# Performance work log

Measured on AMD Instinct MI355X. Metric: run time of the kernel, lower is better.

The kernel has to match this reference:

```python
import jax, jax.numpy as jnp
import numpy as np

COMMITMENT_COST = 0.25


def setup_inputs() -> dict:
    key = jax.random.key(0)
    k1, k2 = jax.random.split(key)
    # z_latents: [B, H, W, D] encoder output latents
    z_latents = jax.random.normal(k1, (128, 32, 32, 64), dtype=jnp.float32)
    # embeddings: [D, K] codebook, uniform init like tf.random_uniform_initializer (default [-0.05, 0.05])
    embeddings = jax.random.uniform(k2, (64, 1024), dtype=jnp.float32, minval=-0.05, maxval=0.05)
    return {"z_latents": z_latents, "embeddings": embeddings}


def reference(z_latents, embeddings):
    d, k = embeddings.shape
    flat = z_latents.reshape(-1, d)  # [N, D]
    # squared L2 distances to each codebook entry: [N, K]
    distances = (
        jnp.sum(flat * flat, axis=1, keepdims=True)
        - 2.0 * (flat @ embeddings)
        + jnp.sum(embeddings * embeddings, axis=0, keepdims=True)
    )
    # argmax(-d) == argmin(d) (both take first occurrence on ties)
    encoding_indices = jnp.argmin(distances, axis=1)  # [N]
    # one-hot @ embeddings.T is just a gather of codebook rows
    quantized = jnp.take(embeddings.T, encoding_indices, axis=0).reshape(z_latents.shape)
    commitment_loss = jnp.mean((jax.lax.stop_gradient(quantized) - z_latents) ** 2)
    embedding_loss = jnp.mean((jax.lax.stop_gradient(z_latents) - quantized) ** 2)
    vq_loss = embedding_loss + COMMITMENT_COST * commitment_loss
    # straight-through estimator
    quantized_st = z_latents + jax.lax.stop_gradient(quantized - z_latents)
    return quantized_st, vq_loss
```

## Files before the change

### kernel.cpp

```cpp
#include <hip/hip_runtime.h>

#pragma clang fp contract(off)

typedef __attribute__((ext_vector_type(8))) short short8;
typedef __attribute__((ext_vector_type(4))) float f32x4;

#define MARGIN 0.02f

static __device__ __forceinline__ unsigned short f2b(float f) {
    union { float f; unsigned u; } x; x.f = f;
    unsigned u = x.u;
    return (unsigned short)((u + 0x7FFFu + ((u >> 16) & 1u)) >> 16);
}

template <int ES>
static __device__ __forceinline__ float np_dist(
    const float* __restrict__ zr, const float* __restrict__ ecol,
    float zn, float en) {
    float c = 0.f;
    #pragma unroll
    for (int i = 0; i < 64; ++i) c = fmaf(zr[i], ecol[i * ES], c);
    float t = zn - 2.f * c;
    return t + en;
}

__global__ __launch_bounds__(256) void vq_prep_t(
    const float* __restrict__ E, float* __restrict__ Et) {
    int t = blockIdx.x * 256 + threadIdx.x;
    int k = t >> 6, d = t & 63;
    Et[t] = E[d * 1024 + k];
}

template <int ES>
__global__ __launch_bounds__(256) void vq_prep(
    const float* __restrict__ src, float* __restrict__ ws_loss,
    float* __restrict__ enorm) {
    int c = blockIdx.x * 256 + threadIdx.x;
    const float* col = src + (ES == 1 ? c * 64 : c);
    float s2 = 0.f;
    #pragma unroll
    for (int d = 0; d < 64; ++d) {
        float v = col[d * ES];
        s2 = fmaf(v, v, s2);
    }
    enorm[c] = s2;
    if (c == 0) *ws_loss = 0.f;
}

template <bool USE_ET>
__global__ __launch_bounds__(256) void vq_main(
    const float* __restrict__ z, const float* __restrict__ E,
    const float* __restrict__ Et, const float* __restrict__ enorm,
    float* __restrict__ ws_loss, float* __restrict__ out) {
    __shared__ unsigned short sB[128 * 64];
    __shared__ float sEn[1024];
    __shared__ float sZn[128];
    __shared__ int sIdx[128];
    __shared__ float sRed[4];

    const int tid = threadIdx.x;
    const int w = tid >> 6;
    const int l = tid & 63;
    const int quad = l >> 4;
    const int m = l & 15;
    const int b = blockIdx.x;

    ((float4*)sEn)[tid] = ((const float4*)enorm)[tid];

    if (tid < 128) {
        const float* zr = z + (b * 128 + tid) * 64;
        float S[16];
        #pragma unroll
        for (int u = 0; u < 16; ++u) { float v = zr[u]; S[u] = v * v; }
        #pragma unroll
        for (int t = 1; t < 4; ++t)
            #pragma unroll
            for (int u = 0; u < 16; ++u) {
                float v = zr[16 * t + u];
                float sq = v * v;
                S[u] = S[u] + sq;
            }
        float R0 = (S[0] + S[4]) + (S[8] + S[12]);
        float R1 = (S[1] + S[5]) + (S[9] + S[13]);
        float R2 = (S[2] + S[6]) + (S[10] + S[14]);
        float R3 = (S[3] + S[7]) + (S[11] + S[15]);
        sZn[tid] = (R0 + R1) + (R2 + R3);
    }

    short8 a[2][2];
    #pragma unroll
    for (int rt = 0; rt < 2; ++rt) {
        const int rowl = w * 32 + rt * 16 + m;
        #pragma unroll
        for (int s = 0; s < 2; ++s) {
            const float* zp = z + (b * 128 + rowl) * 64 + s * 32 + quad * 8;
            union { float4 v; float f[4]; } u0, u1;
            u0.v = *(const float4*)zp;
            u1.v = *(const float4*)(zp + 4);
            short8 av;
            #pragma unroll
            for (int j = 0; j < 4; ++j) av[j] = (short)f2b(u0.f[j]);
            #pragma unroll
            for (int j = 0; j < 4; ++j) av[4 + j] = (short)f2b(u1.f[j]);
            a[rt][s] = av;
        }
    }

    float v1[2][4], v2[2][4];
    int k1[2][4], k2[2][4];
    #pragma unroll
    for (int rt = 0; rt < 2; ++rt)
        #pragma unroll
        for (int r = 0; r < 4; ++r) {
            v1[rt][r] = 3.4e38f; v2[rt][r] = 3.4e38f;
            k1[rt][r] = 0; k2[rt][r] = 0;
        }

    for (int st = 0; st < 8; ++st) {
        #pragma unroll
        for (int i = 0; i < 4; ++i) {
            const int u = tid + i * 256;
            const int d0 = (u & 31) * 2;
            const int cg = u >> 5;
            const float* e0 = E + d0 * 1024 + st * 128 + cg * 4;
            union { float4 v; float f[4]; } va, vb;
            va.v = *(const float4*)e0;
            vb.v = *(const float4*)(e0 + 1024);
            #pragma unroll
            for (int j = 0; j < 4; ++j) {
                const int col = cg * 4 + j;
                const unsigned lo = f2b(va.f[j]);
                const unsigned hi = f2b(vb.f[j]);
                const int gi = col * 8 + ((d0 >> 3) ^ (col & 7));
                *(unsigned*)&sB[gi * 8 + (d0 & 7)] = lo | (hi << 16);
            }
        }
        __syncthreads();

        #pragma unroll
        for (int ct = 0; ct < 8; ++ct) {
            const int c = st * 8 + ct;
            const int colb = (ct * 16 + m) * 8;
            short8 b0 = *(const short8*)&sB[(colb + (quad ^ (m & 7))) * 8];
            short8 b1 = *(const short8*)&sB[(colb + ((4 + quad) ^ (m & 7))) * 8];
            f32x4 acc0 = {0.f, 0.f, 0.f, 0.f};
            f32x4 acc1 = {0.f, 0.f, 0.f, 0.f};
            acc0 = __builtin_amdgcn_mfma_f32_16x16x32_bf16(a[0][0], b0, acc0, 0, 0, 0);
            acc0 = __builtin_amdgcn_mfma_f32_16x16x32_bf16(a[0][1], b1, acc0, 0, 0, 0);
            acc1 = __builtin_amdgcn_mfma_f32_16x16x32_bf16(a[1][0], b0, acc1, 0, 0, 0);
            acc1 = __builtin_amdgcn_mfma_f32_16x16x32_bf16(a[1][1], b1, acc1, 0, 0, 0);
            const float en = sEn[c * 16 + m];
            #pragma unroll
            for (int r = 0; r < 4; ++r) {
                float v0 = fmaf(-2.f, acc0[r], en);
                bool p1 = v0 < v1[0][r];
                bool p2 = v0 < v2[0][r];
                v2[0][r] = p1 ? v1[0][r] : (p2 ? v0 : v2[0][r]);
                k2[0][r] = p1 ? k1[0][r] : (p2 ? c : k2[0][r]);
                v1[0][r] = p1 ? v0 : v1[0][r];
                k1[0][r] = p1 ? c : k1[0][r];
                float w1 = fmaf(-2.f, acc1[r], en);
                bool q1 = w1 < v1[1][r];
                bool q2 = w1 < v2[1][r];
                v2[1][r] = q1 ? v1[1][r] : (q2 ? w1 : v2[1][r]);
                k2[1][r] = q1 ? k1[1][r] : (q2 ? c : k2[1][r]);
                v1[1][r] = q1 ? w1 : v1[1][r];
                k1[1][r] = q1 ? c : k1[1][r];
            }
        }
        __syncthreads();
    }

    float la = 0.f;
    #pragma unroll
    for (int rt = 0; rt < 2; ++rt) {
        #pragma unroll
        for (int r = 0; r < 4; ++r) {
            float vb = v1[rt][r];
            #pragma unroll
            for (int mask = 1; mask <= 8; mask <<= 1)
                vb = fminf(vb, __shfl_xor(vb, mask));
            const int rowl = w * 32 + rt * 16 + quad * 4 + r;
            const float zn = sZn[rowl];
            const float* zr = z + (b * 128 + rowl) * 64;
            float d = 3.4e38f;
            int kk = 0x7fffffff;
            if (v1[rt][r] <= vb + MARGIN) {
                kk = k1[rt][r] * 16 + m;
                d = USE_ET ? np_dist<1>(zr, Et + kk * 64, zn, sEn[kk])
                           : np_dist<1024>(zr, E + kk, zn, sEn[kk]);
            }
            if (v2[rt][r] <= vb + MARGIN) {
                int kc = k2[rt][r] * 16 + m;
                float dd = USE_ET ? np_dist<1>(zr, Et + kc * 64, zn, sEn[kc])
                                  : np_dist<1024>(zr, E + kc, zn, sEn[kc]);
                if (dd < d || (dd == d && kc < kk)) { d = dd; kk = kc; }
            }
            #pragma unroll
            for (int mask = 1; mask <= 8; mask <<= 1) {
                float d2 = __shfl_xor(d, mask);
                int c2 = __shfl_xor(kk, mask);
                bool take = (d2 < d) || (d2 == d && c2 < kk);
                d = take ? d2 : d;
                kk = take ? c2 : kk;
            }
            if (m == 0) {
                sIdx[rowl] = kk;
                la += d;
            }
        }
    }
    __syncthreads();

    {
        const int row_local = w * 32 + (l >> 1);
        const int half = l & 1;
        const int idx = sIdx[row_local];
        union { float s[32]; float4 f[8]; } tmp;
        if (USE_ET) {
            const float4* src = (const float4*)(Et + idx * 64 + half * 32);
            #pragma unroll
            for (int q4 = 0; q4 < 8; ++q4) tmp.f[q4] = src[q4];
        } else {
            #pragma unroll
            for (int dd = 0; dd < 32; ++dd) tmp.s[dd] = E[(half * 32 + dd) * 1024 + idx];
        }
        float4* dst = (float4*)(out + (b * 128 + row_local) * 64 + half * 32);
        #pragma unroll
        for (int q4 = 0; q4 < 8; ++q4) dst[q4] = tmp.f[q4];
    }

    #pragma unroll
    for (int mask = 32; mask >= 1; mask >>= 1) la += __shfl_xor(la, mask);
    if (l == 0) sRed[w] = la;
    __syncthreads();
    if (tid == 0) atomicAdd(ws_loss, sRed[0] + sRed[1] + sRed[2] + sRed[3]);
}

__global__ void vq_final(const float* __restrict__ ws_loss,
                         float* __restrict__ out) {
    out[8388608] = (*ws_loss) * (1.25f / 8388608.f);
}

extern "C" void kernel_launch(void* const* d_in, const int* in_sizes, int n_in,
                              void* d_out, int out_size, void* d_ws, size_t ws_size,
                              hipStream_t stream) {
    const float* z = (const float*)d_in[0];
    const float* E = (const float*)d_in[1];
    float* out = (float*)d_out;

    char* ws = (char*)d_ws;
    float* loss = (float*)ws;
    float* enorm = (float*)(ws + 128);
    float* Et = (float*)(ws + 8192);
    const bool useEt = ws_size >= (size_t)(8192 + 65536 * 4);

    if (useEt) {
        vq_prep_t<<<256, 256, 0, stream>>>(E, Et);
        vq_prep<1><<<4, 256, 0, stream>>>(Et, loss, enorm);
        vq_main<true><<<1024, 256, 0, stream>>>(z, E, Et, enorm, loss, out);
    } else {
        vq_prep<1024><<<4, 256, 0, stream>>>(E, loss, enorm);
        vq_main<false><<<1024, 256, 0, stream>>>(z, E, Et, enorm, loss, out);
    }
    vq_final<<<1, 1, 0, stream>>>(loss, out);
}
```

Before: 174.8 us.

## Precompute swizzled bf16 codebook, double-buffer LDS tiles, pack index into distance bits

A single fused prep kernel now builds the transposed fp32 codebook, the norms, and a pre-swizzled bf16 copy of the codebook. Each main-kernel block then streams the bf16 copy straight into double-buffered shared memory, with the next tile prefetched into registers while MFMAs run. This removes the per-block fp32 load and bf16 conversion and one barrier per stage. The top-2 tracking packs the 6-bit column-tile index into the low mantissa bits of the distance, so fminf and fmed3 replace compare/select chains; this costs a little precision in the candidate screen, which the margin-based exact recheck absorbs. Shared memory doubles for sB, which may lower occupancy.

```diff
diff --git a/kernel.cpp b/kernel.cpp
--- a/kernel.cpp
+++ b/kernel.cpp
@@ -24,35 +24,49 @@
     return t + en;
 }
 
-__global__ __launch_bounds__(256) void vq_prep_t(
-    const float* __restrict__ E, float* __restrict__ Et) {
-    int t = blockIdx.x * 256 + threadIdx.x;
-    int k = t >> 6, d = t & 63;
-    Et[t] = E[d * 1024 + k];
-}
-
-template <int ES>
-__global__ __launch_bounds__(256) void vq_prep(
-    const float* __restrict__ src, float* __restrict__ ws_loss,
-    float* __restrict__ enorm) {
-    int c = blockIdx.x * 256 + threadIdx.x;
-    const float* col = src + (ES == 1 ? c * 64 : c);
-    float s2 = 0.f;
-    #pragma unroll
-    for (int d = 0; d < 64; ++d) {
-        float v = col[d * ES];
-        s2 = fmaf(v, v, s2);
-    }
-    enorm[c] = s2;
-    if (c == 0) *ws_loss = 0.f;
-}
-
-template <bool USE_ET>
+template <bool ET, bool EB>
+__global__ __launch_bounds__(256) void vq_prep_all(
+    const float* __restrict__ E, float* __restrict__ ws_loss,
+    float* __restrict__ enorm, float* __restrict__ Et,
+    unsigned* __restrict__ EbW) {
+    const int t = blockIdx.x * 256 + threadIdx.x;
+    if (ET) {
+        Et[t] = E[(t & 63) * 1024 + (t >> 6)];
+    }
+    if (EB) {
+        if (t < 32768) {
+            const int st = t >> 12;
+            const int r = t & 4095;
+            const int col = r >> 5;
+            const int w = r & 31;
+            const int g = w >> 2;
+            const int d0 = ((g ^ (col & 7)) << 3) | ((w & 3) << 1);
+            const int gc = st * 128 + col;
+            const unsigned lo = f2b(E[d0 * 1024 + gc]);
+            const unsigned hi = f2b(E[(d0 + 1) * 1024 + gc]);
+            EbW[t] = lo | (hi << 16);
+        }
+    }
+    if (t < 1024) {
+        const float* colp = E + t;
+        float s2 = 0.f;
+        #pragma unroll
+        for (int d = 0; d < 64; ++d) {
+            float v = colp[d * 1024];
+            s2 = fmaf(v, v, s2);
+        }
+        enorm[t] = s2;
+        if (t == 0) *ws_loss = 0.f;
+    }
+}
+
+template <bool USE_ET, bool USE_EB>
 __global__ __launch_bounds__(256) void vq_main(
     const float* __restrict__ z, const float* __restrict__ E,
-    const float* __restrict__ Et, const float* __restrict__ enorm,
+    const float* __restrict__ Et, const unsigned short* __restrict__ Eb,
+    const float* __restrict__ enorm,
     float* __restrict__ ws_loss, float* __restrict__ out) {
-    __shared__ unsigned short sB[128 * 64];
+    __shared__ unsigned short sB[2][128 * 64];
     __shared__ float sEn[1024];
     __shared__ float sZn[128];
     __shared__ int sIdx[128];
@@ -106,43 +120,61 @@
         }
     }
 
-    float v1[2][4], v2[2][4];
-    int k1[2][4], k2[2][4];
+    float v1p[2][4], v2p[2][4];
     #pragma unroll
     for (int rt = 0; rt < 2; ++rt)
         #pragma unroll
-        for (int r = 0; r < 4; ++r) {
-            v1[rt][r] = 3.4e38f; v2[rt][r] = 3.4e38f;
-            k1[rt][r] = 0; k2[rt][r] = 0;
-        }
+        for (int r = 0; r < 4; ++r) { v1p[rt][r] = 3.4e38f; v2p[rt][r] = 3.4e38f; }
+
+    short8 nx0, nx1, nx2, nx3;
+    if (USE_EB) {
+        const short8* s0 = (const short8*)Eb;
+        short8* dp = (short8*)sB[0];
+        #pragma unroll
+        for (int i = 0; i < 4; ++i) dp[tid + i * 256] = s0[tid + i * 256];
+        __syncthreads();
+    }
 
     for (int st = 0; st < 8; ++st) {
-        #pragma unroll
-        for (int i = 0; i < 4; ++i) {
-            const int u = tid + i * 256;
-            const int d0 = (u & 31) * 2;
-            const int cg = u >> 5;
-            const float* e0 = E + d0 * 1024 + st * 128 + cg * 4;
-            union { float4 v; float f[4]; } va, vb;
-            va.v = *(const float4*)e0;
-            vb.v = *(const float4*)(e0 + 1024);
-            #pragma unroll
-            for (int j = 0; j < 4; ++j) {
-                const int col = cg * 4 + j;
-                const unsigned lo = f2b(va.f[j]);
-                const unsigned hi = f2b(vb.f[j]);
-                const int gi = col * 8 + ((d0 >> 3) ^ (col & 7));
-                *(unsigned*)&sB[gi * 8 + (d0 & 7)] = lo | (hi << 16);
-            }
-        }
-        __syncthreads();
+        const unsigned short* sBc;
+        if (USE_EB) {
+            if (st < 7) {
+                const short8* sn = (const short8*)(Eb + (st + 1) * 8192);
+                nx0 = sn[tid];
+                nx1 = sn[tid + 256];
+                nx2 = sn[tid + 512];
+                nx3 = sn[tid + 768];
+            }
+            sBc = sB[st & 1];
+        } else {
+            #pragma unroll
+            for (int i = 0; i < 4; ++i) {
+                const int u = tid + i * 256;
+                const int d0 = (u & 31) * 2;
+                const int cg = u >> 5;
+                const float* e0 = E + d0 * 1024 + st * 128 + cg * 4;
+                union { float4 v; float f[4]; } va, vb;
+                va.v = *(const float4*)e0;
+                vb.v = *(const float4*)(e0 + 1024);
+                #pragma unroll
+                for (int j = 0; j < 4; ++j) {
+                    const int col = cg * 4 + j;
+                    const unsigned lo = f2b(va.f[j]);
+                    const unsigned hi = f2b(vb.f[j]);
+                    const int gi = col * 8 + ((d0 >> 3) ^ (col & 7));
+                    *(unsigned*)&sB[0][gi * 8 + (d0 & 7)] = lo | (hi << 16);
+                }
+            }
+            __syncthreads();
+            sBc = sB[0];
+        }
 
         #pragma unroll
         for (int ct = 0; ct < 8; ++ct) {
             const int c = st * 8 + ct;
             const int colb = (ct * 16 + m) * 8;
-            short8 b0 = *(const short8*)&sB[(colb + (quad ^ (m & 7))) * 8];
-            short8 b1 = *(const short8*)&sB[(colb + ((4 + quad) ^ (m & 7))) * 8];
+            short8 b0 = *(const short8*)&sBc[(colb + (quad ^ (m & 7))) * 8];
+            short8 b1 = *(const short8*)&sBc[(colb + ((4 + quad) ^ (m & 7))) * 8];
             f32x4 acc0 = {0.f, 0.f, 0.f, 0.f};
             f32x4 acc1 = {0.f, 0.f, 0.f, 0.f};
             acc0 = __builtin_amdgcn_mfma_f32_16x16x32_bf16(a[0][0], b0, acc0, 0, 0, 0);
@@ -152,23 +184,29 @@
             const float en = sEn[c * 16 + m];
             #pragma unroll
             for (int r = 0; r < 4; ++r) {
-                float v0 = fmaf(-2.f, acc0[r], en);
-                bool p1 = v0 < v1[0][r];
-                bool p2 = v0 < v2[0][r];
-                v2[0][r] = p1 ? v1[0][r] : (p2 ? v0 : v2[0][r]);
-                k2[0][r] = p1 ? k1[0][r] : (p2 ? c : k2[0][r]);
-                v1[0][r] = p1 ? v0 : v1[0][r];
-                k1[0][r] = p1 ? c : k1[0][r];
-                float w1 = fmaf(-2.f, acc1[r], en);
-                bool q1 = w1 < v1[1][r];
-                bool q2 = w1 < v2[1][r];
-                v2[1][r] = q1 ? v1[1][r] : (q2 ? w1 : v2[1][r]);
-                k2[1][r] = q1 ? k1[1][r] : (q2 ? c : k2[1][r]);
-                v1[1][r] = q1 ? w1 : v1[1][r];
-                k1[1][r] = q1 ? c : k1[1][r];
-            }
-        }
-        __syncthreads();
+                float p0 = fmaf(-2.f, acc0[r], en);
+                p0 = __uint_as_float((__float_as_uint(p0) & 0xFFFFFFC0u) | (unsigned)c);
+                v2p[0][r] = __builtin_amdgcn_fmed3f(p0, v1p[0][r], v2p[0][r]);
+                v1p[0][r] = fminf(p0, v1p[0][r]);
+                float p1 = fmaf(-2.f, acc1[r], en);
+                p1 = __uint_as_float((__float_as_uint(p1) & 0xFFFFFFC0u) | (unsigned)c);
+                v2p[1][r] = __builtin_amdgcn_fmed3f(p1, v1p[1][r], v2p[1][r]);
+                v1p[1][r] = fminf(p1, v1p[1][r]);
+            }
+        }
+
+        if (USE_EB) {
+            if (st < 7) {
+                short8* dn = (short8*)sB[(st & 1) ^ 1];
+                dn[tid] = nx0;
+                dn[tid + 256] = nx1;
+                dn[tid + 512] = nx2;
+                dn[tid + 768] = nx3;
+            }
+            __syncthreads();
+        } else {
+            __syncthreads();
+        }
     }
 
     float la = 0.f;
@@ -176,7 +214,8 @@
     for (int rt = 0; rt < 2; ++rt) {
         #pragma unroll
         for (int r = 0; r < 4; ++r) {
-            float vb = v1[rt][r];
+            float pv1 = v1p[rt][r];
+            float vb = pv1;
             #pragma unroll
             for (int mask = 1; mask <= 8; mask <<= 1)
                 vb = fminf(vb, __shfl_xor(vb, mask));
@@ -185,13 +224,14 @@
             const float* zr = z + (b * 128 + rowl) * 64;
             float d = 3.4e38f;
             int kk = 0x7fffffff;
-            if (v1[rt][r] <= vb + MARGIN) {
-                kk = k1[rt][r] * 16 + m;
+            if (pv1 <= vb + MARGIN) {
+                kk = (int)(__float_as_uint(pv1) & 63u) * 16 + m;
                 d = USE_ET ? np_dist<1>(zr, Et + kk * 64, zn, sEn[kk])
                            : np_dist<1024>(zr, E + kk, zn, sEn[kk]);
             }
-            if (v2[rt][r] <= vb + MARGIN) {
-                int kc = k2[rt][r] * 16 + m;
+            float pv2 = v2p[rt][r];
+            if (pv2 <= vb + MARGIN) {
+                int kc = (int)(__float_as_uint(pv2) & 63u) * 16 + m;
                 float dd = USE_ET ? np_dist<1>(zr, Et + kc * 64, zn, sEn[kc])
                                   : np_dist<1024>(zr, E + kc, zn, sEn[kc]);
                 if (dd < d || (dd == d && kc < kk)) { d = dd; kk = kc; }
@@ -252,16 +292,20 @@
     char* ws = (char*)d_ws;
     float* loss = (float*)ws;
     float* enorm = (float*)(ws + 128);
-    float* Et = (float*)(ws + 8192);
-    const bool useEt = ws_size >= (size_t)(8192 + 65536 * 4);
+    unsigned short* Eb = (unsigned short*)(ws + 8192);
+    float* Et = (float*)(ws + 139264);
+    const bool useEb = ws_size >= (size_t)139264;
+    const bool useEt = ws_size >= (size_t)401408;
 
     if (useEt) {
-        vq_prep_t<<<256, 256, 0, stream>>>(E, Et);
-        vq_prep<1><<<4, 256, 0, stream>>>(Et, loss, enorm);
-        vq_main<true><<<1024, 256, 0, stream>>>(z, E, Et, enorm, loss, out);
+        vq_prep_all<true, true><<<256, 256, 0, stream>>>(E, loss, enorm, Et, (unsigned*)Eb);
+        vq_main<true, true><<<1024, 256, 0, stream>>>(z, E, Et, Eb, enorm, loss, out);
+    } else if (useEb) {
+        vq_prep_all<false, true><<<256, 256, 0, stream>>>(E, loss, enorm, Et, (unsigned*)Eb);
+        vq_main<false, true><<<1024, 256, 0, stream>>>(z, E, Et, Eb, enorm, loss, out);
     } else {
-        vq_prep<1024><<<4, 256, 0, stream>>>(E, loss, enorm);
-        vq_main<false><<<1024, 256, 0, stream>>>(z, E, Et, enorm, loss, out);
+        vq_prep_all<false, false><<<256, 256, 0, stream>>>(E, loss, enorm, Et, (unsigned*)Eb);
+        vq_main<false, false><<<1024, 256, 0, stream>>>(z, E, Et, Eb, enorm, loss, out);
     }
     vq_final<<<1, 1, 0, stream>>>(loss, out);
 }
```

Result: faster. 158.4 us (-9.4%).
